# Optimization experiments

Measured on AMD Instinct MI355X. Metric: run time of the kernel, lower is better.

Reference implementation:

```python
import jax, jax.numpy as jnp
import numpy as np

N = 50000          # nodes
E = 400000         # edges
MUL = 32           # multiplicity per irrep
NUM_NEIGHBORS = 8.0
INV_SQRT3 = 1.0 / np.sqrt(3.0)  # w3j(1,1,0) coefficient


def setup_inputs() -> dict:
    key = jax.random.key(0)
    ks = jax.random.split(key, 20)
    inp = {
        # node_input: 32x0e (dim 32) + 32x1o (dim 96) = 128
        "node_input": jax.random.normal(ks[0], (N, 4 * MUL), jnp.float32),
        "node_attr": jnp.ones((N, 1), jnp.float32),           # 1x0e trivial attr
        "edge_src": jax.random.randint(ks[1], (E,), 0, N, jnp.int32),
        "edge_dst": jax.random.randint(ks[2], (E,), 0, N, jnp.int32),
        "edge_attr": jax.random.normal(ks[3], (E, 4), jnp.float32),   # 1x0e + 1x1o
        "edge_scalars": jax.random.normal(ks[4], (E, 16), jnp.float32),
        # FullyConnectedTensorProduct weights (uvw, node_attr has mul 1)
        "w_sc0": jax.random.normal(ks[5], (MUL, MUL), jnp.float32),
        "w_sc1": jax.random.normal(ks[6], (MUL, MUL), jnp.float32),
        "w_lin1_0": jax.random.normal(ks[7], (MUL, MUL), jnp.float32),
        "w_lin1_1": jax.random.normal(ks[8], (MUL, MUL), jnp.float32),
        # radial FC net -> per-edge TP weights (numel = 4*MUL = 128)
        "fc_w1": jax.random.normal(ks[9], (16, 64), jnp.float32),
        "fc_w2": jax.random.normal(ks[10], (64, 4 * MUL), jnp.float32),
        # lin2: irreps_mid (64x0e+64x1o) x attr -> output
        "w_lin2_0": jax.random.normal(ks[11], (2 * MUL, MUL), jnp.float32),
        "w_lin2_1": jax.random.normal(ks[12], (2 * MUL, MUL), jnp.float32),
        # alpha: irreps_mid x attr -> 0e (zero-init in original; small randn for a nontrivial test)
        "w_alpha": 0.1 * jax.random.normal(ks[13], (2 * MUL, 1), jnp.float32),
        # sc_edges: irreps_mid x edge_attr -> edge_attr
        "w_se0a": jax.random.normal(ks[14], (2 * MUL,), jnp.float32),  # mid0e x ea0e -> 0e
        "w_se0b": jax.random.normal(ks[15], (2 * MUL,), jnp.float32),  # mid1o x ea1o -> 0e
        "w_se1a": jax.random.normal(ks[16], (2 * MUL,), jnp.float32),  # mid0e x ea1o -> 1o
        "w_se1b": jax.random.normal(ks[17], (2 * MUL,), jnp.float32),  # mid1o x ea0e -> 1o
    }
    return inp


def reference(node_input, node_attr, edge_src, edge_dst, edge_attr, edge_scalars,
              w_sc0, w_sc1, w_lin1_0, w_lin1_1, fc_w1, fc_w2,
              w_lin2_0, w_lin2_1, w_alpha, w_se0a, w_se0b, w_se1a, w_se1b):
    inv_nn = 1.0 / jnp.sqrt(jnp.asarray(NUM_NEIGHBORS, node_input.dtype))
    n = node_input.shape[0]
    x0 = node_input[:, :MUL]                       # (N, 32)   32x0e
    x1 = node_input[:, MUL:].reshape(n, MUL, 3)    # (N, 32, 3) 32x1o
    a = node_attr                                  # (N, 1)
    s_in = 1.0 / np.sqrt(MUL)                      # FCTP fan-in normalization

    # self-connection: FCTP(input, attr) -> output
    sc0 = (x0 @ w_sc0) * a * s_in
    sc1 = jnp.einsum('num,uw->nwm', x1, w_sc1) * a[:, :, None] * s_in
    node_self = jnp.concatenate([sc0, sc1.reshape(n, 3 * MUL)], axis=1)  # (N, 128)

    # lin1: FCTP(input, attr) -> input irreps
    f0 = (x0 @ w_lin1_0) * a * s_in
    f1 = jnp.einsum('num,uw->nwm', x1, w_lin1_1) * a[:, :, None] * s_in

    # gather source node features per edge
    g0 = f0[edge_src]                              # (E, 32)
    g1 = f1[edge_src]                              # (E, 32, 3)
    ea0 = edge_attr[:, :1]                         # (E, 1)   1x0e
    ea1 = edge_attr[:, 1:]                         # (E, 3)   1x1o

    # radial net -> per-edge TP weights (FullyConnectedNet with sin activation)
    h = jnp.sin(edge_scalars @ fc_w1 * (1.0 / np.sqrt(16.0)))
    w = h @ fc_w2 * (1.0 / np.sqrt(64.0))          # (E, 128)
    wA, wB, wC, wD = jnp.split(w, 4, axis=1)       # each (E, 32)

    # uvu tensor product, 4 instructions
    mA = wA * g0 * ea0                                           # 0e x 0e -> 0e
    mD = wD * jnp.einsum('eum,em->eu', g1, ea1) * INV_SQRT3      # 1o x 1o -> 0e
    mB = (wB * g0)[:, :, None] * ea1[:, None, :]                 # 0e x 1o -> 1o
    mC = (wC[:, :, None] * g1) * ea0[:, :, None]                 # 1o x 0e -> 1o
    mid0 = jnp.concatenate([mA, mD], axis=1)       # (E, 64)  64x0e
    mid1 = jnp.concatenate([mB, mC], axis=1)       # (E, 64, 3) 64x1o

    # scatter-add to destination nodes
    n0 = jax.ops.segment_sum(mid0, edge_dst, num_segments=n) * inv_nn
    n1 = jax.ops.segment_sum(mid1, edge_dst, num_segments=n) * inv_nn

    s_mid = 1.0 / np.sqrt(2 * MUL)
    out0 = (n0 @ w_lin2_0) * a * s_mid
    out1 = jnp.einsum('num,uw->nwm', n1, w_lin2_1) * a[:, :, None] * s_mid
    node_conv = jnp.concatenate([out0, out1.reshape(n, 3 * MUL)], axis=1)

    # alpha gate (sc.output_mask is all ones here, so alpha = 1 - 1 + alpha*1)
    alpha = (n0 @ w_alpha) * a * s_mid             # (N, 1)
    node_conv_out = node_self + alpha * node_conv  # (N, 128)

    # sc_edges: FCTP(mid, edge_attr) -> edge_attr irreps; fan-in = 128 per output
    s_se = 1.0 / np.sqrt(4 * MUL)
    se0 = ((mid0 @ w_se0a) * ea0[:, 0]
           + jnp.einsum('eum,em,u->e', mid1, ea1, w_se0b) * INV_SQRT3) * s_se
    se1 = ((mid0 @ w_se1a)[:, None] * ea1
           + jnp.einsum('eum,u->em', mid1, w_se1b) * ea0) * s_se
    edge_conv_out = edge_attr + jnp.concatenate([se0[:, None], se1], axis=1) * inv_nn

    return node_conv_out, edge_conv_out
```

## Files before the change

### kernel.cpp

```cpp
#include <hip/hip_runtime.h>
#include <math.h>

#define N_NODES 50000
#define E_EDGES 400000
#define NPRE_BLOCKS 6250
#define NHIST_BLOCKS 1563
#define NEDGE_BLOCKS 6250

typedef _Float16 f16x2 __attribute__((ext_vector_type(2)));
typedef _Float16 f16x4 __attribute__((ext_vector_type(4)));
typedef _Float16 f16x8 __attribute__((ext_vector_type(8)));
typedef float    f32x4 __attribute__((ext_vector_type(4)));

static constexpr float S_IN      = 0.17677669529663687f;
static constexpr float S_MID     = 0.125f;
static constexpr float S_SE      = 0.08838834764831843f;
static constexpr float INV_NN    = 0.35355339059327373f;
static constexpr float INV_SQRT3 = 0.5773502691896258f;
static constexpr float FC1_S     = 0.25f;
static constexpr float FC2_S     = 0.125f;

#define WAVE_LDS_FENCE() asm volatile("s_waitcnt lgkmcnt(0)" ::: "memory")

__device__ inline float wave_reduce_dpp(float v) {
    int x;
    x = __builtin_amdgcn_update_dpp(0, __float_as_int(v), 0x111, 0xf, 0xf, true); v += __int_as_float(x);
    x = __builtin_amdgcn_update_dpp(0, __float_as_int(v), 0x112, 0xf, 0xf, true); v += __int_as_float(x);
    x = __builtin_amdgcn_update_dpp(0, __float_as_int(v), 0x114, 0xf, 0xf, true); v += __int_as_float(x);
    x = __builtin_amdgcn_update_dpp(0, __float_as_int(v), 0x118, 0xf, 0xf, true); v += __int_as_float(x);
    x = __builtin_amdgcn_update_dpp(0, __float_as_int(v), 0x142, 0xa, 0xf, true); v += __int_as_float(x);
    x = __builtin_amdgcn_update_dpp(0, __float_as_int(v), 0x143, 0xc, 0xf, true); v += __int_as_float(x);
    return __int_as_float(__builtin_amdgcn_readlane(__float_as_int(v), 63));
}

__global__ __launch_bounds__(256) void pre_hist_kernel(
    const float* __restrict__ node_input, const float* __restrict__ node_attr,
    const float* __restrict__ w_sc0, const float* __restrict__ w_sc1,
    const float* __restrict__ w_lin1_0, const float* __restrict__ w_lin1_1,
    float* __restrict__ out_self, _Float16* __restrict__ ws_h,
    const int* __restrict__ edge_dst, int* __restrict__ counts,
    const float* __restrict__ edge_scalars, _Float16* __restrict__ ES_h,
    float* __restrict__ nacc)
{
    const int t = threadIdx.x;
    if (blockIdx.x >= NPRE_BLOCKS) {
        const int e = (blockIdx.x - NPRE_BLOCKS) * 256 + t;
        if (e < E_EDGES) {
            atomicAdd(&counts[edge_dst[e]], 1);
            const float4* s4 = (const float4*)edge_scalars + (size_t)e * 4;
            _Float16* dp = ES_h + (size_t)e * 16;
            #pragma unroll
            for (int i = 0; i < 4; ++i) {
                const float4 v = s4[i];
                f16x4 p = {(_Float16)v.x, (_Float16)v.y, (_Float16)v.z, (_Float16)v.w};
                *(f16x4*)&dp[i * 4] = p;
            }
        }
        return;
    }
    const int n0 = blockIdx.x * 8;
    __shared__ __align__(16) float sx[8 * 128];
    __shared__ float sa[8];
    {
        const int k = t >> 5, q = t & 31;
        const float4 v = ((const float4*)(node_input + (size_t)n0 * 128))[t];
        if (q < 8) {
            *(float4*)&sx[k * 128 + q * 4] = v;
        } else {
            const int base = q * 4 - 32;
            const float vv[4] = {v.x, v.y, v.z, v.w};
            #pragma unroll
            for (int j = 0; j < 4; ++j) {
                const int uj = (base + j) / 3, mj = (base + j) % 3;
                sx[k * 128 + 32 + mj * 32 + uj] = vv[j];
            }
        }
    }
    {
        float4* nz = (float4*)(nacc + (size_t)n0 * 256);
        const float4 z4 = {0.f, 0.f, 0.f, 0.f};
        nz[t] = z4; nz[t + 256] = z4;
    }
    if (t < 8) sa[t] = node_attr[n0 + t];
    __syncthreads();

    const int half = t >> 7;
    const int idx  = t & 127;
    float wcol[32];
    int xoff = 0;
    if (idx < 32) {
        const float* __restrict__ W = half ? w_lin1_0 : w_sc0;
        #pragma unroll
        for (int u = 0; u < 32; ++u) wcol[u] = W[u * 32 + idx];
    } else {
        const float* __restrict__ W = half ? w_lin1_1 : w_sc1;
        const int j = idx - 32;
        const int w = j / 3; const int m = j % 3;
        xoff = 32 + m * 32;
        #pragma unroll
        for (int u = 0; u < 32; ++u) wcol[u] = W[u * 32 + w];
    }
    #pragma unroll
    for (int k = 0; k < 8; ++k) {
        const float* xb = sx + k * 128 + xoff;
        float acc = 0.f;
        #pragma unroll
        for (int u4 = 0; u4 < 8; ++u4) {
            const f32x4 xv = *(const f32x4*)&xb[u4 * 4];
            acc += xv[0] * wcol[u4 * 4 + 0];
            acc += xv[1] * wcol[u4 * 4 + 1];
            acc += xv[2] * wcol[u4 * 4 + 2];
            acc += xv[3] * wcol[u4 * 4 + 3];
        }
        const float v = acc * sa[k] * S_IN;
        if (half) ws_h[(size_t)(n0 + k) * 128 + idx] = (_Float16)v;
        else      out_self[(size_t)(n0 + k) * 128 + idx] = v;
    }
}

__global__ __launch_bounds__(1024) void scan_block_kernel(
    const int* __restrict__ counts, int* __restrict__ cursor, int* __restrict__ bsum,
    const float* __restrict__ fc_w1, const float* __restrict__ fc_w2,
    const float* __restrict__ w_se0a, const float* __restrict__ w_se0b,
    const float* __restrict__ w_se1a, const float* __restrict__ w_se1b,
    _Float16* __restrict__ W2T_g, _Float16* __restrict__ W1T_g,
    _Float16* __restrict__ BT_g)
{
    const int t = threadIdx.x;
    if (blockIdx.x == 49) {
        for (int u = t; u < 8192; u += 1024) {
            const int k = u >> 7, c = u & 127;
            W2T_g[c * 72 + k] = (_Float16)fc_w2[u];
        }
        {
            W2T_g[(t >> 3) * 72 + 64 + (t & 7)] = (_Float16)0.f;
        }
        {
            const int j = t >> 4, k = t & 15;
            W1T_g[t] = (_Float16)fc_w1[k * 64 + j];
        }
        for (int u = t; u < 2112; u += 1024) BT_g[u] = (_Float16)0.f;
        __syncthreads();
        if (t < 256) {
            const int uu = t & 63, p = t >> 6;
            const float ev = (p == 0) ? w_se0a[uu] : w_se1b[uu];
            const float ov = (p == 0) ? w_se1a[uu] : w_se0b[uu];
            BT_g[(2 * p) * 264 + 4 * uu + p]     = (_Float16)ev;
            BT_g[(2 * p + 1) * 264 + 4 * uu + p] = (_Float16)ov;
        }
        return;
    }
    const int idx = blockIdx.x * 1024 + t;
    const int c   = (idx < N_NODES) ? counts[idx] : 0;
    int v = c, x;
    x = __builtin_amdgcn_update_dpp(0, v, 0x111, 0xf, 0xf, true); v += x;
    x = __builtin_amdgcn_update_dpp(0, v, 0x112, 0xf, 0xf, true); v += x;
    x = __builtin_amdgcn_update_dpp(0, v, 0x114, 0xf, 0xf, true); v += x;
    x = __builtin_amdgcn_update_dpp(0, v, 0x118, 0xf, 0xf, true); v += x;
    x = __builtin_amdgcn_update_dpp(0, v, 0x142, 0xa, 0xf, true); v += x;
    x = __builtin_amdgcn_update_dpp(0, v, 0x143, 0xc, 0xf, true); v += x;
    __shared__ int swv[16], sex[16];
    const int wid = t >> 6;
    if ((t & 63) == 63) swv[wid] = v;
    __syncthreads();
    if (t < 16) {
        int a = 0;
        for (int j = 0; j < t; ++j) a += swv[j];
        sex[t] = a;
        if (t == 15) bsum[blockIdx.x] = a + swv[15];
    }
    __syncthreads();
    if (idx < N_NODES) cursor[idx] = v - c + sex[wid];
}

__global__ __launch_bounds__(1024) void scan_fixup_kernel(
    int* __restrict__ cursor, const int* __restrict__ bsum)
{
    __shared__ int boff_s;
    const int t = threadIdx.x;
    if (t < 64) {
        int v = (t < (int)blockIdx.x) ? bsum[t] : 0;
        #pragma unroll
        for (int off = 32; off >= 1; off >>= 1) v += __shfl_down(v, off, 64);
        if (t == 0) boff_s = v;
    }
    __syncthreads();
    const int idx = blockIdx.x * 1024 + t;
    if (idx < N_NODES) cursor[idx] += boff_s;
}

__global__ __launch_bounds__(256) void scatter_kernel(
    const int* __restrict__ edge_dst, int* __restrict__ cursor,
    int* __restrict__ sorted_eid)
{
    const int e = blockIdx.x * 256 + threadIdx.x;
    if (e < E_EDGES) {
        const int p = atomicAdd(&cursor[edge_dst[e]], 1);
        sorted_eid[p] = e;
    }
}

__global__ __launch_bounds__(256, 4) void edge_kernel(
    const _Float16* __restrict__ ws_h,
    const int* __restrict__ edge_src, const int* __restrict__ edge_dst,
    const float* __restrict__ edge_attr, const _Float16* __restrict__ ES_h,
    const _Float16* __restrict__ W2T_g, const _Float16* __restrict__ W1T_g,
    const _Float16* __restrict__ BT_g,
    const int* __restrict__ sorted_eid,
    float* __restrict__ nacc, float* __restrict__ edge_out)
{
    __shared__ __align__(16) _Float16 sArena[17536];
    __shared__ __align__(16) float sEA[64 * 4];
    __shared__ __align__(16) float sDep[4][36];
    __shared__ int sSRC[64];
    __shared__ int sDST[64];
    __shared__ int sEID[64];

    _Float16* __restrict__ sHT   = sArena;
    _Float16* __restrict__ sWt   = sArena + 4608;
    _Float16* __restrict__ sMidA = sArena + 13312;

    const int t    = threadIdx.x;
    const int lane = t & 63;
    const int wv   = t >> 6;
    const int quad = lane >> 4;
    const int mm   = lane & 15;

    const int orig = blockIdx.x;
    const int xcd  = orig & 7;
    constexpr int q = NEDGE_BLOCKS >> 3, r = NEDGE_BLOCKS & 7;
    const int bid = (xcd < r ? xcd * (q + 1) : r * (q + 1) + (xcd - r) * q) + (orig >> 3);
    const int e0 = bid * 64;
    const int eb = wv * 16;

    f16x8 a_w1[4];
    f16x8 b_es = {};
    if (quad < 2) {
        const int myeid = sorted_eid[e0 + eb + mm];
        b_es = *(const f16x8*)&ES_h[(size_t)myeid * 16 + quad * 8];
        #pragma unroll
        for (int jt = 0; jt < 4; ++jt)
            a_w1[jt] = *(const f16x8*)&W1T_g[(jt * 16 + mm) * 16 + quad * 8];
    } else {
        #pragma unroll
        for (int jt = 0; jt < 4; ++jt) a_w1[jt] = (f16x8){};
    }
    f16x8 bt[8];
    #pragma unroll
    for (int ks = 0; ks < 8; ++ks)
        bt[ks] = *(const f16x8*)&BT_g[(mm & 7) * 264 + ks * 32 + quad * 8];

    if (lane < 16) {
        const int eid = sorted_eid[e0 + eb + lane];
        sEID[eb + lane] = eid;
        sSRC[eb + lane] = edge_src[eid];
        sDST[eb + lane] = edge_dst[eid];
        *(float4*)&sEA[(eb + lane) * 4] = ((const float4*)edge_attr)[eid];
    }
    WAVE_LDS_FENCE();

    const bool hi = lane >= 32;
    const int  u  = lane - 32;
    const int idxA = hi ? (32 + 3 * u) : lane;
    const int idxB = hi ? (33 + 3 * u) : lane;
    const int idxC = hi ? (34 + 3 * u) : lane;
    const int col1 = hi ? (96 + u) : lane;
    const int col2 = hi ? (64 + u) : (32 + lane);

    float ga[4][4], gb[4][4], gc[4][4];
    #pragma unroll
    for (int b = 0; b < 4; ++b)
        #pragma unroll
        for (int i = 0; i < 4; ++i) {
            const _Float16* fr = ws_h + (size_t)sSRC[eb + b * 4 + i] * 128;
            ga[b][i] = (float)fr[idxA];
            gb[b][i] = (float)fr[idxB];
            gc[b][i] = (float)fr[idxC];
        }
    asm volatile("" ::: "memory");

    #pragma unroll
    for (int jt = 0; jt < 4; ++jt) {
        f32x4 d = {0.f, 0.f, 0.f, 0.f};
        d = __builtin_amdgcn_mfma_f32_16x16x32_f16(a_w1[jt], b_es, d, 0, 0, 0);
        f16x4 hv;
        hv[0] = (_Float16)__sinf(d[0] * FC1_S);
        hv[1] = (_Float16)__sinf(d[1] * FC1_S);
        hv[2] = (_Float16)__sinf(d[2] * FC1_S);
        hv[3] = (_Float16)__sinf(d[3] * FC1_S);
        *(f16x4*)&sHT[(eb + mm) * 72 + jt * 16 + quad * 4] = hv;
    }
    WAVE_LDS_FENCE();

    f32x4 dacc[8];
    {
        const f16x8 b_lo = *(const f16x8*)&sHT[(eb + mm) * 72 + quad * 8];
        const f16x8 b_hi = *(const f16x8*)&sHT[(eb + mm) * 72 + 32 + quad * 8];
        #pragma unroll
        for (int ct = 0; ct < 8; ++ct) {
            const f16x8 a_lo = *(const f16x8*)&W2T_g[(ct * 16 + mm) * 72 + quad * 8];
            const f16x8 a_hi = *(const f16x8*)&W2T_g[(ct * 16 + mm) * 72 + 32 + quad * 8];
            f32x4 d = {0.f, 0.f, 0.f, 0.f};
            d = __builtin_amdgcn_mfma_f32_16x16x32_f16(a_lo, b_lo, d, 0, 0, 0);
            d = __builtin_amdgcn_mfma_f32_16x16x32_f16(a_hi, b_hi, d, 0, 0, 0);
            dacc[ct] = d;
        }
    }

    #pragma unroll
    for (int ct = 0; ct < 8; ++ct) {
        f16x4 v;
        v[0] = (_Float16)(dacc[ct][0] * FC2_S);
        v[1] = (_Float16)(dacc[ct][1] * FC2_S);
        v[2] = (_Float16)(dacc[ct][2] * FC2_S);
        v[3] = (_Float16)(dacc[ct][3] * FC2_S);
        *(f16x4*)&sWt[(eb + mm) * 136 + ct * 16 + quad * 4] = v;
    }
    WAVE_LDS_FENCE();

    int   cur = -1;
    float am0 = 0.f, axx = 0.f, ayy = 0.f, azz = 0.f;
    _Float16* __restrict__ myA = sMidA + wv * 1056;
    const _Float16* __restrict__ arow = myA + (mm & 3) * 264;

    #pragma unroll
    for (int b = 0; b < 4; ++b) {
        float w1b[4], w2b[4];
        #pragma unroll
        for (int i = 0; i < 4; ++i) {
            w1b[i] = (float)sWt[(eb + b * 4 + i) * 136 + col1];
            w2b[i] = (float)sWt[(eb + b * 4 + i) * 136 + col2];
        }
        #pragma unroll
        for (int i = 0; i < 4; ++i) {
            const int el  = eb + b * 4 + i;
            const int dst = sDST[el];
            const float ea0 = sEA[el * 4 + 0];
            const float e1x = sEA[el * 4 + 1];
            const float e1y = sEA[el * 4 + 2];
            const float e1z = sEA[el * 4 + 3];
            const float w1v = w1b[i];
            const float w2v = w2b[i];

            float mid0, m1x, m1y, m1z;
            if (!hi) {
                mid0 = w1v * ga[b][i] * ea0;
                const float wbg = w2v * ga[b][i];
                m1x = wbg * e1x; m1y = wbg * e1y; m1z = wbg * e1z;
            } else {
                const float dot = ga[b][i] * e1x + gb[b][i] * e1y + gc[b][i] * e1z;
                mid0 = w1v * dot * INV_SQRT3;
                const float wce = w2v * ea0;
                m1x = wce * ga[b][i]; m1y = wce * gb[b][i]; m1z = wce * gc[b][i];
            }

            if (dst != cur) {
                if (cur >= 0) {
                    float* np_ = nacc + (size_t)cur * 256;
                    atomicAdd(np_ + lane, am0);
                    atomicAdd(np_ + 64 + lane, axx);
                    atomicAdd(np_ + 128 + lane, ayy);
                    atomicAdd(np_ + 192 + lane, azz);
                }
                cur = dst; am0 = axx = ayy = azz = 0.f;
            }
            am0 += mid0; axx += m1x; ayy += m1y; azz += m1z;

            f16x4 mv;
            mv[0] = (_Float16)mid0; mv[1] = (_Float16)m1x;
            mv[2] = (_Float16)m1y;  mv[3] = (_Float16)m1z;
            *(f16x4*)&myA[i * 264 + 4 * lane] = mv;
        }

        f32x4 d = {0.f, 0.f, 0.f, 0.f};
        #pragma unroll
        for (int ks = 0; ks < 8; ++ks) {
            const f16x8 a = *(const f16x8*)&arow[ks * 32 + quad * 8];
            d = __builtin_amdgcn_mfma_f32_16x16x32_f16(a, bt[ks], d, 0, 0, 0);
        }
        if (lane < 8) {
            float4 f4; f4.x = d[0]; f4.y = d[1]; f4.z = d[2]; f4.w = d[3];
            *(float4*)&sDep[wv][lane * 4] = f4;
        }
        if (lane < 4) {
            const int el = eb + b * 4 + lane;
            const float c0 = sDep[wv][ 0 + lane], c1 = sDep[wv][ 4 + lane];
            const float c2 = sDep[wv][ 8 + lane], c3 = sDep[wv][12 + lane];
            const float c4 = sDep[wv][16 + lane], c5 = sDep[wv][20 + lane];
            const float c6 = sDep[wv][24 + lane], c7 = sDep[wv][28 + lane];
            const float ea0 = sEA[el * 4 + 0];
            const float e1x = sEA[el * 4 + 1];
            const float e1y = sEA[el * 4 + 2];
            const float e1z = sEA[el * 4 + 3];
            const float s0 = c0 * ea0 + (c3 * e1x + c5 * e1y + c7 * e1z) * INV_SQRT3;
            float4 o;
            o.x = ea0 + s0 * S_SE * INV_NN;
            o.y = e1x + (c1 * e1x + c2 * ea0) * S_SE * INV_NN;
            o.z = e1y + (c1 * e1y + c4 * ea0) * S_SE * INV_NN;
            o.w = e1z + (c1 * e1z + c6 * ea0) * S_SE * INV_NN;
            *(float4*)&edge_out[(size_t)sEID[el] * 4] = o;
        }
    }
    if (cur >= 0) {
        float* np_ = nacc + (size_t)cur * 256;
        atomicAdd(np_ + lane, am0);
        atomicAdd(np_ + 64 + lane, axx);
        atomicAdd(np_ + 128 + lane, ayy);
        atomicAdd(np_ + 192 + lane, azz);
    }
}

__global__ __launch_bounds__(128) void node_post_kernel(
    const float* __restrict__ nacc, const float* __restrict__ node_attr,
    const float* __restrict__ w_lin2_0, const float* __restrict__ w_lin2_1,
    const float* __restrict__ w_alpha, float* __restrict__ out)
{
    const int n0 = blockIdx.x * 8, t = threadIdx.x;
    __shared__ __align__(16) float sn[8 * 256];
    __shared__ float salpha[8];
    const float4* src = (const float4*)(nacc + (size_t)n0 * 256);
    #pragma unroll
    for (int i = 0; i < 4; ++i) ((float4*)sn)[t + i * 128] = src[t + i * 128];
    __syncthreads();

    if (t < 64) {
        const float wa = w_alpha[t];
        #pragma unroll
        for (int k = 0; k < 8; ++k) {
            const float r = wave_reduce_dpp(sn[k * 256 + t] * wa);
            if (t == 0) salpha[k] = r;
        }
    }
    __syncthreads();

    float wcol[64];
    int xoff = 0;
    if (t < 32) {
        #pragma unroll
        for (int u = 0; u < 64; ++u) wcol[u] = w_lin2_0[u * 32 + t];
    } else {
        const int j = t - 32; const int w = j / 3; const int m = j % 3;
        xoff = 64 + m * 64;
        #pragma unroll
        for (int u = 0; u < 64; ++u) wcol[u] = w_lin2_1[u * 32 + w];
    }
    #pragma unroll
    for (int k = 0; k < 8; ++k) {
        const float* xb = sn + k * 256 + xoff;
        float acc = 0.f;
        #pragma unroll
        for (int u4 = 0; u4 < 16; ++u4) {
            const f32x4 xv = *(const f32x4*)&xb[u4 * 4];
            acc += xv[0] * wcol[u4 * 4 + 0];
            acc += xv[1] * wcol[u4 * 4 + 1];
            acc += xv[2] * wcol[u4 * 4 + 2];
            acc += xv[3] * wcol[u4 * 4 + 3];
        }
        const float a  = node_attr[n0 + k];
        const float sc = a * S_MID * INV_NN;
        const size_t o = (size_t)(n0 + k) * 128 + t;
        out[o] = out[o] + (salpha[k] * sc) * (acc * sc);
    }
}

extern "C" void kernel_launch(void* const* d_in, const int* in_sizes, int n_in,
                              void* d_out, int out_size, void* d_ws, size_t ws_size,
                              hipStream_t stream)
{
    const float* node_input   = (const float*)d_in[0];
    const float* node_attr    = (const float*)d_in[1];
    const int*   edge_src     = (const int*)d_in[2];
    const int*   edge_dst     = (const int*)d_in[3];
    const float* edge_attr    = (const float*)d_in[4];
    const float* edge_scalars = (const float*)d_in[5];
    const float* w_sc0        = (const float*)d_in[6];
    const float* w_sc1        = (const float*)d_in[7];
    const float* w_lin1_0     = (const float*)d_in[8];
    const float* w_lin1_1     = (const float*)d_in[9];
    const float* fc_w1        = (const float*)d_in[10];
    const float* fc_w2        = (const float*)d_in[11];
    const float* w_lin2_0     = (const float*)d_in[12];
    const float* w_lin2_1     = (const float*)d_in[13];
    const float* w_alpha      = (const float*)d_in[14];
    const float* w_se0a       = (const float*)d_in[15];
    const float* w_se0b       = (const float*)d_in[16];
    const float* w_se1a       = (const float*)d_in[17];
    const float* w_se1b       = (const float*)d_in[18];

    float* out      = (float*)d_out;
    float* edge_out = out + (size_t)N_NODES * 128;

    _Float16* ws_h = (_Float16*)d_ws;
    _Float16* ES_h = ws_h + (size_t)N_NODES * 128;
    float* nacc   = (float*)((char*)d_ws + (size_t)N_NODES * 128 * 4);
    int*   counts = (int*)(nacc + (size_t)N_NODES * 256);
    int*   cursor = counts + N_NODES;
    int*   sid    = cursor + N_NODES;
    int*   bsum   = sid + E_EDGES;
    _Float16* W2T_g = (_Float16*)(bsum + 64);
    _Float16* W1T_g = W2T_g + 9216;
    _Float16* BT_g  = W1T_g + 1024;

    hipMemsetAsync(counts, 0, N_NODES * sizeof(int), stream);

    pre_hist_kernel<<<NPRE_BLOCKS + NHIST_BLOCKS, 256, 0, stream>>>(
        node_input, node_attr, w_sc0, w_sc1, w_lin1_0, w_lin1_1, out, ws_h,
        edge_dst, counts, edge_scalars, ES_h, nacc);

    scan_block_kernel<<<50, 1024, 0, stream>>>(counts, cursor, bsum,
        fc_w1, fc_w2, w_se0a, w_se0b, w_se1a, w_se1b, W2T_g, W1T_g, BT_g);
    scan_fixup_kernel<<<49, 1024, 0, stream>>>(cursor, bsum);
    scatter_kernel<<<(E_EDGES + 255) / 256, 256, 0, stream>>>(edge_dst, cursor, sid);

    edge_kernel<<<NEDGE_BLOCKS, 256, 0, stream>>>(
        ws_h, edge_src, edge_dst, edge_attr, ES_h, W2T_g, W1T_g, BT_g,
        sid, nacc, edge_out);

    node_post_kernel<<<N_NODES / 8, 128, 0, stream>>>(
        nacc, node_attr, w_lin2_0, w_lin2_1, w_alpha, out);
}
```

Before: 369.2 us.

## Fuse counting-sort stages into one persistent kernel with grid barriers

Replaces the memset, histogram, block scan, scan fixup and scatter launches with a single 50-block persistent sort kernel that uses atomic-counter grid barriers between phases. Weight preprocessing moves into an extra block of the pre kernel. The edge kernel now keeps per-edge src/dst/eid/attr in registers and broadcasts them with shuffles, which shrinks LDS and allows 5 blocks per CU. This cuts launch overhead and LDS pressure. In exchange the histogram and scatter run on only 50 blocks, and the spin barrier depends on all blocks being co-resident.

```diff
diff --git a/kernel.cpp b/kernel.cpp
--- a/kernel.cpp
+++ b/kernel.cpp
@@ -6,6 +6,7 @@
 #define NPRE_BLOCKS 6250
 #define NHIST_BLOCKS 1563
 #define NEDGE_BLOCKS 6250
+#define NSORT_BLOCKS 50
 
 typedef _Float16 f16x2 __attribute__((ext_vector_type(2)));
 typedef _Float16 f16x4 __attribute__((ext_vector_type(4)));
@@ -33,20 +34,58 @@
     return __int_as_float(__builtin_amdgcn_readlane(__float_as_int(v), 63));
 }
 
+__device__ inline void gsync(int* cnt, int target) {
+    __syncthreads();
+    if (threadIdx.x == 0) {
+        __hip_atomic_fetch_add(cnt, 1, __ATOMIC_ACQ_REL, __HIP_MEMORY_SCOPE_AGENT);
+        while (__hip_atomic_load(cnt, __ATOMIC_ACQUIRE, __HIP_MEMORY_SCOPE_AGENT) < target)
+            __builtin_amdgcn_s_sleep(8);
+    }
+    __syncthreads();
+    __threadfence();
+}
+
 __global__ __launch_bounds__(256) void pre_hist_kernel(
     const float* __restrict__ node_input, const float* __restrict__ node_attr,
     const float* __restrict__ w_sc0, const float* __restrict__ w_sc1,
     const float* __restrict__ w_lin1_0, const float* __restrict__ w_lin1_1,
     float* __restrict__ out_self, _Float16* __restrict__ ws_h,
-    const int* __restrict__ edge_dst, int* __restrict__ counts,
     const float* __restrict__ edge_scalars, _Float16* __restrict__ ES_h,
-    float* __restrict__ nacc)
+    float* __restrict__ nacc,
+    const float* __restrict__ fc_w1, const float* __restrict__ fc_w2,
+    const float* __restrict__ w_se0a, const float* __restrict__ w_se0b,
+    const float* __restrict__ w_se1a, const float* __restrict__ w_se1b,
+    _Float16* __restrict__ W2T_g, _Float16* __restrict__ W1T_g,
+    _Float16* __restrict__ BT_g, int* __restrict__ sync_cnt)
 {
     const int t = threadIdx.x;
+    if (blockIdx.x == 0 && t == 0) *sync_cnt = 0;
+    if (blockIdx.x == NPRE_BLOCKS + NHIST_BLOCKS) {
+        for (int u = t; u < 8192; u += 256) {
+            const int k = u >> 7, c = u & 127;
+            W2T_g[c * 72 + k] = (_Float16)fc_w2[u];
+        }
+        for (int u = t; u < 1024; u += 256) {
+            W2T_g[(u >> 3) * 72 + 64 + (u & 7)] = (_Float16)0.f;
+        }
+        for (int u = t; u < 1024; u += 256) {
+            const int j = u >> 4, k = u & 15;
+            W1T_g[u] = (_Float16)fc_w1[k * 64 + j];
+        }
+        for (int u = t; u < 2112; u += 256) BT_g[u] = (_Float16)0.f;
+        __syncthreads();
+        {
+            const int uu = t & 63, p = t >> 6;
+            const float ev = (p == 0) ? w_se0a[uu] : w_se1b[uu];
+            const float ov = (p == 0) ? w_se1a[uu] : w_se0b[uu];
+            BT_g[(2 * p) * 264 + 4 * uu + p]     = (_Float16)ev;
+            BT_g[(2 * p + 1) * 264 + 4 * uu + p] = (_Float16)ov;
+        }
+        return;
+    }
     if (blockIdx.x >= NPRE_BLOCKS) {
         const int e = (blockIdx.x - NPRE_BLOCKS) * 256 + t;
         if (e < E_EDGES) {
-            atomicAdd(&counts[edge_dst[e]], 1);
             const float4* s4 = (const float4*)edge_scalars + (size_t)e * 4;
             _Float16* dp = ES_h + (size_t)e * 16;
             #pragma unroll
@@ -118,40 +157,22 @@
     }
 }
 
-__global__ __launch_bounds__(1024) void scan_block_kernel(
-    const int* __restrict__ counts, int* __restrict__ cursor, int* __restrict__ bsum,
-    const float* __restrict__ fc_w1, const float* __restrict__ fc_w2,
-    const float* __restrict__ w_se0a, const float* __restrict__ w_se0b,
-    const float* __restrict__ w_se1a, const float* __restrict__ w_se1b,
-    _Float16* __restrict__ W2T_g, _Float16* __restrict__ W1T_g,
-    _Float16* __restrict__ BT_g)
+__global__ __launch_bounds__(1024) void sort_kernel(
+    const int* __restrict__ edge_dst, int* __restrict__ counts,
+    int* __restrict__ cursor, int* __restrict__ bsum,
+    int* __restrict__ sorted_eid, int* __restrict__ sync_cnt)
 {
-    const int t = threadIdx.x;
-    if (blockIdx.x == 49) {
-        for (int u = t; u < 8192; u += 1024) {
-            const int k = u >> 7, c = u & 127;
-            W2T_g[c * 72 + k] = (_Float16)fc_w2[u];
-        }
-        {
-            W2T_g[(t >> 3) * 72 + 64 + (t & 7)] = (_Float16)0.f;
-        }
-        {
-            const int j = t >> 4, k = t & 15;
-            W1T_g[t] = (_Float16)fc_w1[k * 64 + j];
-        }
-        for (int u = t; u < 2112; u += 1024) BT_g[u] = (_Float16)0.f;
-        __syncthreads();
-        if (t < 256) {
-            const int uu = t & 63, p = t >> 6;
-            const float ev = (p == 0) ? w_se0a[uu] : w_se1b[uu];
-            const float ov = (p == 0) ? w_se1a[uu] : w_se0b[uu];
-            BT_g[(2 * p) * 264 + 4 * uu + p]     = (_Float16)ev;
-            BT_g[(2 * p + 1) * 264 + 4 * uu + p] = (_Float16)ov;
-        }
-        return;
-    }
-    const int idx = blockIdx.x * 1024 + t;
-    const int c   = (idx < N_NODES) ? counts[idx] : 0;
+    const int t = threadIdx.x, b = blockIdx.x;
+    const int idx = b * 1024 + t;
+
+    if (idx < N_NODES) counts[idx] = 0;
+    gsync(sync_cnt, 1 * NSORT_BLOCKS);
+
+    for (int e = idx; e < E_EDGES; e += NSORT_BLOCKS * 1024)
+        atomicAdd(&counts[edge_dst[e]], 1);
+    gsync(sync_cnt, 2 * NSORT_BLOCKS);
+
+    const int c = (idx < N_NODES) ? counts[idx] : 0;
     int v = c, x;
     x = __builtin_amdgcn_update_dpp(0, v, 0x111, 0xf, 0xf, true); v += x;
     x = __builtin_amdgcn_update_dpp(0, v, 0x112, 0xf, 0xf, true); v += x;
@@ -167,40 +188,30 @@
         int a = 0;
         for (int j = 0; j < t; ++j) a += swv[j];
         sex[t] = a;
-        if (t == 15) bsum[blockIdx.x] = a + swv[15];
-    }
-    __syncthreads();
-    if (idx < N_NODES) cursor[idx] = v - c + sex[wid];
-}
-
-__global__ __launch_bounds__(1024) void scan_fixup_kernel(
-    int* __restrict__ cursor, const int* __restrict__ bsum)
-{
+        if (t == 15) bsum[b] = a + swv[15];
+    }
+    __syncthreads();
+    const int myexc = v - c + sex[wid];
+    gsync(sync_cnt, 3 * NSORT_BLOCKS);
+
     __shared__ int boff_s;
-    const int t = threadIdx.x;
     if (t < 64) {
-        int v = (t < (int)blockIdx.x) ? bsum[t] : 0;
-        #pragma unroll
-        for (int off = 32; off >= 1; off >>= 1) v += __shfl_down(v, off, 64);
-        if (t == 0) boff_s = v;
-    }
-    __syncthreads();
-    const int idx = blockIdx.x * 1024 + t;
-    if (idx < N_NODES) cursor[idx] += boff_s;
-}
-
-__global__ __launch_bounds__(256) void scatter_kernel(
-    const int* __restrict__ edge_dst, int* __restrict__ cursor,
-    int* __restrict__ sorted_eid)
-{
-    const int e = blockIdx.x * 256 + threadIdx.x;
-    if (e < E_EDGES) {
+        int vv = (t < b) ? bsum[t] : 0;
+        #pragma unroll
+        for (int off = 32; off >= 1; off >>= 1) vv += __shfl_down(vv, off, 64);
+        if (t == 0) boff_s = vv;
+    }
+    __syncthreads();
+    if (idx < N_NODES) cursor[idx] = myexc + boff_s;
+    gsync(sync_cnt, 4 * NSORT_BLOCKS);
+
+    for (int e = idx; e < E_EDGES; e += NSORT_BLOCKS * 1024) {
         const int p = atomicAdd(&cursor[edge_dst[e]], 1);
         sorted_eid[p] = e;
     }
 }
 
-__global__ __launch_bounds__(256, 4) void edge_kernel(
+__global__ __launch_bounds__(256, 5) void edge_kernel(
     const _Float16* __restrict__ ws_h,
     const int* __restrict__ edge_src, const int* __restrict__ edge_dst,
     const float* __restrict__ edge_attr, const _Float16* __restrict__ ES_h,
@@ -209,16 +220,11 @@
     const int* __restrict__ sorted_eid,
     float* __restrict__ nacc, float* __restrict__ edge_out)
 {
-    __shared__ __align__(16) _Float16 sArena[17536];
-    __shared__ __align__(16) float sEA[64 * 4];
+    __shared__ __align__(16) _Float16 sArena[13056];
     __shared__ __align__(16) float sDep[4][36];
-    __shared__ int sSRC[64];
-    __shared__ int sDST[64];
-    __shared__ int sEID[64];
-
-    _Float16* __restrict__ sHT   = sArena;
-    _Float16* __restrict__ sWt   = sArena + 4608;
-    _Float16* __restrict__ sMidA = sArena + 13312;
+
+    _Float16* __restrict__ sHT = sArena;
+    _Float16* __restrict__ sWt = sArena + 4608;
 
     const int t    = threadIdx.x;
     const int lane = t & 63;
@@ -233,10 +239,19 @@
     const int e0 = bid * 64;
     const int eb = wv * 16;
 
+    int eidreg = 0, srcreg = 0, dstreg = 0;
+    float4 ear = {0.f, 0.f, 0.f, 0.f};
+    if (lane < 16) {
+        eidreg = sorted_eid[e0 + eb + lane];
+        srcreg = edge_src[eidreg];
+        dstreg = edge_dst[eidreg];
+        ear    = ((const float4*)edge_attr)[eidreg];
+    }
+
     f16x8 a_w1[4];
     f16x8 b_es = {};
     if (quad < 2) {
-        const int myeid = sorted_eid[e0 + eb + mm];
+        const int myeid = __shfl(eidreg, mm);
         b_es = *(const f16x8*)&ES_h[(size_t)myeid * 16 + quad * 8];
         #pragma unroll
         for (int jt = 0; jt < 4; ++jt)
@@ -249,15 +264,6 @@
     #pragma unroll
     for (int ks = 0; ks < 8; ++ks)
         bt[ks] = *(const f16x8*)&BT_g[(mm & 7) * 264 + ks * 32 + quad * 8];
-
-    if (lane < 16) {
-        const int eid = sorted_eid[e0 + eb + lane];
-        sEID[eb + lane] = eid;
-        sSRC[eb + lane] = edge_src[eid];
-        sDST[eb + lane] = edge_dst[eid];
-        *(float4*)&sEA[(eb + lane) * 4] = ((const float4*)edge_attr)[eid];
-    }
-    WAVE_LDS_FENCE();
 
     const bool hi = lane >= 32;
     const int  u  = lane - 32;
@@ -272,7 +278,8 @@
     for (int b = 0; b < 4; ++b)
         #pragma unroll
         for (int i = 0; i < 4; ++i) {
-            const _Float16* fr = ws_h + (size_t)sSRC[eb + b * 4 + i] * 128;
+            const int s = __shfl(srcreg, b * 4 + i);
+            const _Float16* fr = ws_h + (size_t)s * 128;
             ga[b][i] = (float)fr[idxA];
             gb[b][i] = (float)fr[idxB];
             gc[b][i] = (float)fr[idxC];
@@ -314,13 +321,13 @@
         v[1] = (_Float16)(dacc[ct][1] * FC2_S);
         v[2] = (_Float16)(dacc[ct][2] * FC2_S);
         v[3] = (_Float16)(dacc[ct][3] * FC2_S);
-        *(f16x4*)&sWt[(eb + mm) * 136 + ct * 16 + quad * 4] = v;
+        *(f16x4*)&sWt[(eb + mm) * 132 + ct * 16 + quad * 4] = v;
     }
     WAVE_LDS_FENCE();
 
     int   cur = -1;
     float am0 = 0.f, axx = 0.f, ayy = 0.f, azz = 0.f;
-    _Float16* __restrict__ myA = sMidA + wv * 1056;
+    _Float16* __restrict__ myA = sArena + wv * 1152;
     const _Float16* __restrict__ arow = myA + (mm & 3) * 264;
 
     #pragma unroll
@@ -328,17 +335,17 @@
         float w1b[4], w2b[4];
         #pragma unroll
         for (int i = 0; i < 4; ++i) {
-            w1b[i] = (float)sWt[(eb + b * 4 + i) * 136 + col1];
-            w2b[i] = (float)sWt[(eb + b * 4 + i) * 136 + col2];
+            w1b[i] = (float)sWt[(eb + b * 4 + i) * 132 + col1];
+            w2b[i] = (float)sWt[(eb + b * 4 + i) * 132 + col2];
         }
         #pragma unroll
         for (int i = 0; i < 4; ++i) {
-            const int el  = eb + b * 4 + i;
-            const int dst = sDST[el];
-            const float ea0 = sEA[el * 4 + 0];
-            const float e1x = sEA[el * 4 + 1];
-            const float e1y = sEA[el * 4 + 2];
-            const float e1z = sEA[el * 4 + 3];
+            const int el = b * 4 + i;
+            const int dst = __shfl(dstreg, el);
+            const float ea0 = __shfl(ear.x, el);
+            const float e1x = __shfl(ear.y, el);
+            const float e1y = __shfl(ear.z, el);
+            const float e1z = __shfl(ear.w, el);
             const float w1v = w1b[i];
             const float w2v = w2b[i];
 
@@ -382,23 +389,23 @@
             float4 f4; f4.x = d[0]; f4.y = d[1]; f4.z = d[2]; f4.w = d[3];
             *(float4*)&sDep[wv][lane * 4] = f4;
         }
+        const int oeid = __shfl(eidreg, b * 4 + (lane & 3));
+        const float oea0 = __shfl(ear.x, b * 4 + (lane & 3));
+        const float oe1x = __shfl(ear.y, b * 4 + (lane & 3));
+        const float oe1y = __shfl(ear.z, b * 4 + (lane & 3));
+        const float oe1z = __shfl(ear.w, b * 4 + (lane & 3));
         if (lane < 4) {
-            const int el = eb + b * 4 + lane;
             const float c0 = sDep[wv][ 0 + lane], c1 = sDep[wv][ 4 + lane];
             const float c2 = sDep[wv][ 8 + lane], c3 = sDep[wv][12 + lane];
             const float c4 = sDep[wv][16 + lane], c5 = sDep[wv][20 + lane];
             const float c6 = sDep[wv][24 + lane], c7 = sDep[wv][28 + lane];
-            const float ea0 = sEA[el * 4 + 0];
-            const float e1x = sEA[el * 4 + 1];
-            const float e1y = sEA[el * 4 + 2];
-            const float e1z = sEA[el * 4 + 3];
-            const float s0 = c0 * ea0 + (c3 * e1x + c5 * e1y + c7 * e1z) * INV_SQRT3;
+            const float s0 = c0 * oea0 + (c3 * oe1x + c5 * oe1y + c7 * oe1z) * INV_SQRT3;
             float4 o;
-            o.x = ea0 + s0 * S_SE * INV_NN;
-            o.y = e1x + (c1 * e1x + c2 * ea0) * S_SE * INV_NN;
-            o.z = e1y + (c1 * e1y + c4 * ea0) * S_SE * INV_NN;
-            o.w = e1z + (c1 * e1z + c6 * ea0) * S_SE * INV_NN;
-            *(float4*)&edge_out[(size_t)sEID[el] * 4] = o;
+            o.x = oea0 + s0 * S_SE * INV_NN;
+            o.y = oe1x + (c1 * oe1x + c2 * oea0) * S_SE * INV_NN;
+            o.z = oe1y + (c1 * oe1y + c4 * oea0) * S_SE * INV_NN;
+            o.w = oe1z + (c1 * oe1z + c6 * oea0) * S_SE * INV_NN;
+            *(float4*)&edge_out[(size_t)oeid * 4] = o;
         }
     }
     if (cur >= 0) {
@@ -500,17 +507,16 @@
     _Float16* W2T_g = (_Float16*)(bsum + 64);
     _Float16* W1T_g = W2T_g + 9216;
     _Float16* BT_g  = W1T_g + 1024;
-
-    hipMemsetAsync(counts, 0, N_NODES * sizeof(int), stream);
-
-    pre_hist_kernel<<<NPRE_BLOCKS + NHIST_BLOCKS, 256, 0, stream>>>(
+    int* sync_cnt   = (int*)(BT_g + 2112);
+
+    pre_hist_kernel<<<NPRE_BLOCKS + NHIST_BLOCKS + 1, 256, 0, stream>>>(
         node_input, node_attr, w_sc0, w_sc1, w_lin1_0, w_lin1_1, out, ws_h,
-        edge_dst, counts, edge_scalars, ES_h, nacc);
-
-    scan_block_kernel<<<50, 1024, 0, stream>>>(counts, cursor, bsum,
-        fc_w1, fc_w2, w_se0a, w_se0b, w_se1a, w_se1b, W2T_g, W1T_g, BT_g);
-    scan_fixup_kernel<<<49, 1024, 0, stream>>>(cursor, bsum);
-    scatter_kernel<<<(E_EDGES + 255) / 256, 256, 0, stream>>>(edge_dst, cursor, sid);
+        edge_scalars, ES_h, nacc,
+        fc_w1, fc_w2, w_se0a, w_se0b, w_se1a, w_se1b, W2T_g, W1T_g, BT_g,
+        sync_cnt);
+
+    sort_kernel<<<NSORT_BLOCKS, 1024, 0, stream>>>(
+        edge_dst, counts, cursor, bsum, sid, sync_cnt);
 
     edge_kernel<<<NEDGE_BLOCKS, 256, 0, stream>>>(
         ws_h, edge_src, edge_dst, edge_attr, ES_h, W2T_g, W1T_g, BT_g,
```

New measurement: 638.4 us. 72.9% more time.

## Cut edge kernel LDS and registers to raise occupancy to 5 blocks

Applied to the files above, without the earlier changes.

Per-edge metadata (eid, src, dst, edge_attr) now stays in registers and is broadcast with wave shuffles instead of being staged in LDS. The mid-tensor buffer reuses the arena space after the hidden activations are consumed, and the weight row stride shrinks, so LDS per block drops. The gathered source features are double-buffered over two batches instead of four, and the BT operand is reloaded from global each step rather than held in registers, both to free VGPRs. Launch bounds ask for 5 blocks per SIMD. The cost is extra shuffle and global/L1 traffic and less latency hiding per wave.

```diff
diff --git a/kernel.cpp b/kernel.cpp
--- a/kernel.cpp
+++ b/kernel.cpp
@@ -200,7 +200,7 @@
     }
 }
 
-__global__ __launch_bounds__(256, 4) void edge_kernel(
+__global__ __launch_bounds__(256, 5) void edge_kernel(
     const _Float16* __restrict__ ws_h,
     const int* __restrict__ edge_src, const int* __restrict__ edge_dst,
     const float* __restrict__ edge_attr, const _Float16* __restrict__ ES_h,
@@ -209,16 +209,11 @@
     const int* __restrict__ sorted_eid,
     float* __restrict__ nacc, float* __restrict__ edge_out)
 {
-    __shared__ __align__(16) _Float16 sArena[17536];
-    __shared__ __align__(16) float sEA[64 * 4];
+    __shared__ __align__(16) _Float16 sArena[13056];
     __shared__ __align__(16) float sDep[4][36];
-    __shared__ int sSRC[64];
-    __shared__ int sDST[64];
-    __shared__ int sEID[64];
-
-    _Float16* __restrict__ sHT   = sArena;
-    _Float16* __restrict__ sWt   = sArena + 4608;
-    _Float16* __restrict__ sMidA = sArena + 13312;
+
+    _Float16* __restrict__ sHT = sArena;
+    _Float16* __restrict__ sWt = sArena + 4608;
 
     const int t    = threadIdx.x;
     const int lane = t & 63;
@@ -233,10 +228,19 @@
     const int e0 = bid * 64;
     const int eb = wv * 16;
 
+    int eidreg = 0, srcreg = 0, dstreg = 0;
+    float4 ear = {0.f, 0.f, 0.f, 0.f};
+    if (lane < 16) {
+        eidreg = sorted_eid[e0 + eb + lane];
+        srcreg = edge_src[eidreg];
+        dstreg = edge_dst[eidreg];
+        ear    = ((const float4*)edge_attr)[eidreg];
+    }
+
     f16x8 a_w1[4];
     f16x8 b_es = {};
     if (quad < 2) {
-        const int myeid = sorted_eid[e0 + eb + mm];
+        const int myeid = __shfl(eidreg, mm);
         b_es = *(const f16x8*)&ES_h[(size_t)myeid * 16 + quad * 8];
         #pragma unroll
         for (int jt = 0; jt < 4; ++jt)
@@ -245,19 +249,6 @@
         #pragma unroll
         for (int jt = 0; jt < 4; ++jt) a_w1[jt] = (f16x8){};
     }
-    f16x8 bt[8];
-    #pragma unroll
-    for (int ks = 0; ks < 8; ++ks)
-        bt[ks] = *(const f16x8*)&BT_g[(mm & 7) * 264 + ks * 32 + quad * 8];
-
-    if (lane < 16) {
-        const int eid = sorted_eid[e0 + eb + lane];
-        sEID[eb + lane] = eid;
-        sSRC[eb + lane] = edge_src[eid];
-        sDST[eb + lane] = edge_dst[eid];
-        *(float4*)&sEA[(eb + lane) * 4] = ((const float4*)edge_attr)[eid];
-    }
-    WAVE_LDS_FENCE();
 
     const bool hi = lane >= 32;
     const int  u  = lane - 32;
@@ -267,12 +258,13 @@
     const int col1 = hi ? (96 + u) : lane;
     const int col2 = hi ? (64 + u) : (32 + lane);
 
-    float ga[4][4], gb[4][4], gc[4][4];
-    #pragma unroll
-    for (int b = 0; b < 4; ++b)
+    float ga[2][4], gb[2][4], gc[2][4];
+    #pragma unroll
+    for (int b = 0; b < 2; ++b)
         #pragma unroll
         for (int i = 0; i < 4; ++i) {
-            const _Float16* fr = ws_h + (size_t)sSRC[eb + b * 4 + i] * 128;
+            const int s = __shfl(srcreg, b * 4 + i);
+            const _Float16* fr = ws_h + (size_t)s * 128;
             ga[b][i] = (float)fr[idxA];
             gb[b][i] = (float)fr[idxB];
             gc[b][i] = (float)fr[idxC];
@@ -314,44 +306,46 @@
         v[1] = (_Float16)(dacc[ct][1] * FC2_S);
         v[2] = (_Float16)(dacc[ct][2] * FC2_S);
         v[3] = (_Float16)(dacc[ct][3] * FC2_S);
-        *(f16x4*)&sWt[(eb + mm) * 136 + ct * 16 + quad * 4] = v;
+        *(f16x4*)&sWt[(eb + mm) * 132 + ct * 16 + quad * 4] = v;
     }
     WAVE_LDS_FENCE();
 
     int   cur = -1;
     float am0 = 0.f, axx = 0.f, ayy = 0.f, azz = 0.f;
-    _Float16* __restrict__ myA = sMidA + wv * 1056;
+    _Float16* __restrict__ myA = sArena + wv * 1152;
     const _Float16* __restrict__ arow = myA + (mm & 3) * 264;
+    const _Float16* __restrict__ btrow = BT_g + (mm & 7) * 264;
 
     #pragma unroll
     for (int b = 0; b < 4; ++b) {
+        const int sl = b & 1;
         float w1b[4], w2b[4];
         #pragma unroll
         for (int i = 0; i < 4; ++i) {
-            w1b[i] = (float)sWt[(eb + b * 4 + i) * 136 + col1];
-            w2b[i] = (float)sWt[(eb + b * 4 + i) * 136 + col2];
+            w1b[i] = (float)sWt[(eb + b * 4 + i) * 132 + col1];
+            w2b[i] = (float)sWt[(eb + b * 4 + i) * 132 + col2];
         }
         #pragma unroll
         for (int i = 0; i < 4; ++i) {
-            const int el  = eb + b * 4 + i;
-            const int dst = sDST[el];
-            const float ea0 = sEA[el * 4 + 0];
-            const float e1x = sEA[el * 4 + 1];
-            const float e1y = sEA[el * 4 + 2];
-            const float e1z = sEA[el * 4 + 3];
+            const int el = b * 4 + i;
+            const int dst = __shfl(dstreg, el);
+            const float ea0 = __shfl(ear.x, el);
+            const float e1x = __shfl(ear.y, el);
+            const float e1y = __shfl(ear.z, el);
+            const float e1z = __shfl(ear.w, el);
             const float w1v = w1b[i];
             const float w2v = w2b[i];
 
             float mid0, m1x, m1y, m1z;
             if (!hi) {
-                mid0 = w1v * ga[b][i] * ea0;
-                const float wbg = w2v * ga[b][i];
+                mid0 = w1v * ga[sl][i] * ea0;
+                const float wbg = w2v * ga[sl][i];
                 m1x = wbg * e1x; m1y = wbg * e1y; m1z = wbg * e1z;
             } else {
-                const float dot = ga[b][i] * e1x + gb[b][i] * e1y + gc[b][i] * e1z;
+                const float dot = ga[sl][i] * e1x + gb[sl][i] * e1y + gc[sl][i] * e1z;
                 mid0 = w1v * dot * INV_SQRT3;
                 const float wce = w2v * ea0;
-                m1x = wce * ga[b][i]; m1y = wce * gb[b][i]; m1z = wce * gc[b][i];
+                m1x = wce * ga[sl][i]; m1y = wce * gb[sl][i]; m1z = wce * gc[sl][i];
             }
 
             if (dst != cur) {
@@ -372,33 +366,46 @@
             *(f16x4*)&myA[i * 264 + 4 * lane] = mv;
         }
 
+        if (b < 2) {
+            #pragma unroll
+            for (int i = 0; i < 4; ++i) {
+                const int s = __shfl(srcreg, (b + 2) * 4 + i);
+                const _Float16* fr = ws_h + (size_t)s * 128;
+                ga[sl][i] = (float)fr[idxA];
+                gb[sl][i] = (float)fr[idxB];
+                gc[sl][i] = (float)fr[idxC];
+            }
+            asm volatile("" ::: "memory");
+        }
+
         f32x4 d = {0.f, 0.f, 0.f, 0.f};
         #pragma unroll
         for (int ks = 0; ks < 8; ++ks) {
-            const f16x8 a = *(const f16x8*)&arow[ks * 32 + quad * 8];
-            d = __builtin_amdgcn_mfma_f32_16x16x32_f16(a, bt[ks], d, 0, 0, 0);
+            const f16x8 a  = *(const f16x8*)&arow[ks * 32 + quad * 8];
+            const f16x8 bb = *(const f16x8*)&btrow[ks * 32 + quad * 8];
+            d = __builtin_amdgcn_mfma_f32_16x16x32_f16(a, bb, d, 0, 0, 0);
         }
         if (lane < 8) {
             float4 f4; f4.x = d[0]; f4.y = d[1]; f4.z = d[2]; f4.w = d[3];
             *(float4*)&sDep[wv][lane * 4] = f4;
         }
+        const int oeid = __shfl(eidreg, b * 4 + (lane & 3));
+        const float oea0 = __shfl(ear.x, b * 4 + (lane & 3));
+        const float oe1x = __shfl(ear.y, b * 4 + (lane & 3));
+        const float oe1y = __shfl(ear.z, b * 4 + (lane & 3));
+        const float oe1z = __shfl(ear.w, b * 4 + (lane & 3));
         if (lane < 4) {
-            const int el = eb + b * 4 + lane;
             const float c0 = sDep[wv][ 0 + lane], c1 = sDep[wv][ 4 + lane];
             const float c2 = sDep[wv][ 8 + lane], c3 = sDep[wv][12 + lane];
             const float c4 = sDep[wv][16 + lane], c5 = sDep[wv][20 + lane];
             const float c6 = sDep[wv][24 + lane], c7 = sDep[wv][28 + lane];
-            const float ea0 = sEA[el * 4 + 0];
-            const float e1x = sEA[el * 4 + 1];
-            const float e1y = sEA[el * 4 + 2];
-            const float e1z = sEA[el * 4 + 3];
-            const float s0 = c0 * ea0 + (c3 * e1x + c5 * e1y + c7 * e1z) * INV_SQRT3;
+            const float s0 = c0 * oea0 + (c3 * oe1x + c5 * oe1y + c7 * oe1z) * INV_SQRT3;
             float4 o;
-            o.x = ea0 + s0 * S_SE * INV_NN;
-            o.y = e1x + (c1 * e1x + c2 * ea0) * S_SE * INV_NN;
-            o.z = e1y + (c1 * e1y + c4 * ea0) * S_SE * INV_NN;
-            o.w = e1z + (c1 * e1z + c6 * ea0) * S_SE * INV_NN;
-            *(float4*)&edge_out[(size_t)sEID[el] * 4] = o;
+            o.x = oea0 + s0 * S_SE * INV_NN;
+            o.y = oe1x + (c1 * oe1x + c2 * oea0) * S_SE * INV_NN;
+            o.z = oe1y + (c1 * oe1y + c4 * oea0) * S_SE * INV_NN;
+            o.w = oe1z + (c1 * oe1z + c6 * oea0) * S_SE * INV_NN;
+            *(float4*)&edge_out[(size_t)oeid * 4] = o;
         }
     }
     if (cur >= 0) {
```

Result: no change. 373.2 us (+1.1%).
